# Optimization experiments

Measured on AMD Instinct MI355X. Metric: run time of the kernel, lower is better.

## Reference

```python
import jax, jax.numpy as jnp
import numpy as np

TEMP = 0.05
ALPHA = 0.1
EPS = 1e-12


def setup_inputs() -> dict:
    key = jax.random.key(0)
    k1, k2, k3, k4 = jax.random.split(key, 4)
    bs, emb_dim, n_class, n_aux = 16384, 512, 2000, 5
    features = jax.random.normal(k1, (bs, emb_dim), dtype=jnp.float32)
    word_embed = jax.random.normal(k2, (n_class, emb_dim), dtype=jnp.float32)
    label = jax.random.randint(k3, (bs,), 0, n_class)
    aux = jax.random.randint(k4, (bs, n_aux), 0, n_class)
    return {"features": features, "word_embed": word_embed, "label": label, "aux": aux}


def _cosine_logits(features, word_embed):
    # F.normalize(x, dim=-1): x / max(||x||, eps)
    f = features / jnp.maximum(jnp.linalg.norm(features, axis=-1, keepdims=True), EPS)
    w = word_embed / jnp.maximum(jnp.linalg.norm(word_embed, axis=-1, keepdims=True), EPS)
    return jnp.matmul(f, w.T) / TEMP  # (bs, n_class)


def reference(features, word_embed, label, aux):
    pred = _cosine_logits(features, word_embed)
    lse = jax.nn.logsumexp(pred, axis=1)                                  # log sum exp per row
    tgt = jnp.take_along_axis(pred, label[:, None], axis=1)[:, 0]         # pred[i, target[i]]
    # normal cross entropy: mean_i(-pred[i,t_i] + log sum exp(pred[i]))
    loss_normal = jnp.mean(-tgt + lse)
    # label-smoothing CE: -(1-a)*pred[i,t_i] + lse - (a/n_aux)*sum_j pred[i, aux[i,j]]
    single_alpha = ALPHA / aux.shape[-1]
    aux_logits = jnp.take_along_axis(pred, aux, axis=1)                   # (bs, n_aux)
    loss_ls = jnp.mean(-(1.0 - ALPHA) * tgt + lse - single_alpha * jnp.sum(aux_logits, axis=1))
    loss = 0.5 * (loss_normal + loss_ls)
    acc = jnp.mean((jnp.argmax(pred, axis=1) == label).astype(jnp.float32))
    return loss, acc
```

## Files before the change

kernel.cpp:

```cpp
#include <hip/hip_runtime.h>
#include <hip/hip_bf16.h>
#include <stdint.h>

#define BS   16384
#define NC   2000
#define NCP  2048
#define EMB  512
#define NAUX 5
#define NCHUNK 32
#define GBLK 4096

typedef __bf16 bf16x8 __attribute__((ext_vector_type(8)));
typedef float  f32x4  __attribute__((ext_vector_type(4)));

__global__ __launch_bounds__(256) void norm_kernel(
    const float* __restrict__ feat, const float* __restrict__ wemb,
    __bf16* __restrict__ fn, __bf16* __restrict__ wn)
{
    const int sub = threadIdx.x & 15;
    const int row = blockIdx.x * 16 + (threadIdx.x >> 4);

    if (row >= BS + NC) {
        bf16x8 z = {};
        bf16x8* d = (bf16x8*)(wn + (size_t)(row - BS) * EMB) + sub * 4;
        #pragma unroll
        for (int i = 0; i < 4; ++i) d[i] = z;
        return;
    }
    const float* src;
    __bf16* dst;
    if (row < BS) { src = feat + (size_t)row * EMB;        dst = fn + (size_t)row * EMB; }
    else          { src = wemb + (size_t)(row - BS) * EMB; dst = wn + (size_t)(row - BS) * EMB; }

    const float4* s4 = (const float4*)src + sub * 8;
    float4 x[8];
    float ss = 0.f;
    #pragma unroll
    for (int i = 0; i < 8; ++i) {
        x[i] = s4[i];
        ss += x[i].x * x[i].x + x[i].y * x[i].y + x[i].z * x[i].z + x[i].w * x[i].w;
    }
    #pragma unroll
    for (int m = 1; m < 16; m <<= 1) ss += __shfl_xor(ss, m, 64);
    const float scale = 1.0f / fmaxf(sqrtf(ss), 1e-12f);

    bf16x8* d = (bf16x8*)dst + sub * 4;
    #pragma unroll
    for (int i = 0; i < 4; ++i) {
        bf16x8 o;
        o[0] = (__bf16)(x[2*i].x   * scale); o[1] = (__bf16)(x[2*i].y   * scale);
        o[2] = (__bf16)(x[2*i].z   * scale); o[3] = (__bf16)(x[2*i].w   * scale);
        o[4] = (__bf16)(x[2*i+1].x * scale); o[5] = (__bf16)(x[2*i+1].y * scale);
        o[6] = (__bf16)(x[2*i+1].z * scale); o[7] = (__bf16)(x[2*i+1].w * scale);
        d[i] = o;
    }
}

__global__ __launch_bounds__(256) void main_kernel(
    const __bf16* __restrict__ fn, const __bf16* __restrict__ wn,
    float* __restrict__ es_part, unsigned* __restrict__ key_part)
{
    __shared__ __align__(16) __bf16 As[128 * 64];
    __shared__ __align__(16) __bf16 Bs[128 * 64];

    const int tid   = threadIdx.x;
    const int lane  = tid & 63;
    const int l15   = lane & 15;
    const int quad  = lane >> 4;
    const int wv    = tid >> 6;
    const int wvM   = wv >> 1;
    const int wvN   = wv & 1;
    const int xcd   = blockIdx.x & 7;
    const int j     = blockIdx.x >> 3;
    const int mTile = xcd * 16 + (j >> 4);
    const int nTile = j & 15;

    const __bf16* fbase = fn + (size_t)mTile * 128 * EMB;
    const __bf16* wbase = wn + (size_t)nTile * 128 * EMB;

    const int sRowIn = lane >> 3;
    const int sChunk = (lane & 7) ^ sRowIn;
    f32x4 acc[4][4] = {};

    for (int kk = 0; kk < EMB; kk += 64) {
        __syncthreads();
        #pragma unroll
        for (int p = 0; p < 4; ++p) {
            const int slot = wv * 4 + p;
            const size_t goff = (size_t)(slot * 8 + sRowIn) * EMB + kk + sChunk * 8;
            __builtin_amdgcn_global_load_lds(
                (const __attribute__((address_space(1))) void*)(fbase + goff),
                (__attribute__((address_space(3))) void*)(As + slot * 512), 16, 0, 0);
            __builtin_amdgcn_global_load_lds(
                (const __attribute__((address_space(1))) void*)(wbase + goff),
                (__attribute__((address_space(3))) void*)(Bs + slot * 512), 16, 0, 0);
        }
        __builtin_amdgcn_s_waitcnt(0);
        __syncthreads();

        #pragma unroll
        for (int kc = 0; kc < 2; ++kc) {
            bf16x8 aF[4], bF[4];
            #pragma unroll
            for (int i = 0; i < 4; ++i) {
                const int ar = wvM * 64 + i * 16 + l15;
                const int br = wvN * 64 + i * 16 + l15;
                const int ca = ((kc * 4 + quad) ^ (ar & 7)) * 8;
                const int cb = ((kc * 4 + quad) ^ (br & 7)) * 8;
                aF[i] = *(const bf16x8*)(As + ar * 64 + ca);
                bF[i] = *(const bf16x8*)(Bs + br * 64 + cb);
            }
            #pragma unroll
            for (int mi = 0; mi < 4; ++mi)
                #pragma unroll
                for (int ni = 0; ni < 4; ++ni)
                    acc[mi][ni] = __builtin_amdgcn_mfma_f32_16x16x32_bf16(
                        aF[mi], bF[ni], acc[mi][ni], 0, 0, 0);
        }
    }

    const float C20 = 28.853900817779268f;
    const int chunk = nTile * 2 + wvN;
    #pragma unroll
    for (int mi = 0; mi < 4; ++mi) {
        float    es[4] = {0.f, 0.f, 0.f, 0.f};
        unsigned km[4] = {0u, 0u, 0u, 0u};
        #pragma unroll
        for (int ni = 0; ni < 4; ++ni) {
            const int col = nTile * 128 + wvN * 64 + ni * 16 + l15;
            const unsigned colenc = 2047u - (unsigned)col;
            const bool valid = (col < NC);
            #pragma unroll
            for (int r = 0; r < 4; ++r) {
                float v = valid ? acc[mi][ni][r] : -3.0f;
                es[r] += exp2f((v - 1.0f) * C20);
                unsigned u = __float_as_uint(v);
                unsigned k = u ^ (unsigned)(((int)u >> 31) | 0x80000000);
                unsigned pk = (k & 0xFFFFF800u) | colenc;
                km[r] = pk > km[r] ? pk : km[r];
            }
        }
        #pragma unroll
        for (int r = 0; r < 4; ++r) {
            #pragma unroll
            for (int m = 1; m < 16; m <<= 1) {
                es[r] += __shfl_xor(es[r], m, 64);
                unsigned x = __shfl_xor(km[r], m, 64);
                km[r] = x > km[r] ? x : km[r];
            }
        }
        if (l15 == 0) {
            #pragma unroll
            for (int r = 0; r < 4; ++r) {
                const int row = mTile * 128 + wvM * 64 + mi * 16 + quad * 4 + r;
                es_part [chunk * BS + row] = es[r];
                key_part[chunk * BS + row] = km[r];
            }
        }
    }
}

__global__ __launch_bounds__(256) void gather_fin_kernel(
    const __bf16* __restrict__ fn, const __bf16* __restrict__ wn,
    const int* __restrict__ label, const int* __restrict__ aux,
    const float* __restrict__ es_part, const unsigned* __restrict__ key_part,
    float* __restrict__ blkpart)
{
    const int lane = threadIdx.x & 63;
    const int wv   = threadIdx.x >> 6;
    const int row  = blockIdx.x * 4 + wv;

    bf16x8 f8 = *((const bf16x8*)fn + (size_t)row * (EMB / 8) + lane);
    float fv[8];
    #pragma unroll
    for (int j = 0; j < 8; ++j) fv[j] = (float)f8[j];

    const int lab = label[row];
    int cols[6];
    cols[0] = lab;
    #pragma unroll
    for (int j = 0; j < NAUX; ++j) cols[j + 1] = aux[row * NAUX + j];

    float res[6];
    #pragma unroll
    for (int c = 0; c < 6; ++c) {
        bf16x8 w8 = *((const bf16x8*)wn + (size_t)cols[c] * (EMB / 8) + lane);
        float d = 0.f;
        #pragma unroll
        for (int j = 0; j < 8; ++j) d += fv[j] * (float)w8[j];
        #pragma unroll
        for (int m = 1; m < 64; m <<= 1) d += __shfl_xor(d, m, 64);
        res[c] = d;
    }
    const float tgt  = res[0] * 20.0f;
    const float auxs = (res[1] + res[2] + res[3] + res[4] + res[5]) * 20.0f;

    const int c = lane & 31;
    float    es = es_part [c * BS + row];
    unsigned k  = key_part[c * BS + row];
    #pragma unroll
    for (int m = 1; m < 32; m <<= 1) {
        es += __shfl_xor(es, m, 64);
        unsigned x = __shfl_xor(k, m, 64);
        k = x > k ? x : k;
    }
    const int amax = 2047 - (int)(k & 0x7FFu);
    const float loss = 20.0f + logf(es) - 0.95f * tgt - 0.01f * auxs;
    const float acc  = (amax == lab) ? 1.0f : 0.0f;

    __shared__ float sl[4], sa[4];
    if (lane == 0) { sl[wv] = loss; sa[wv] = acc; }
    __syncthreads();
    if (threadIdx.x == 0) {
        blkpart[blockIdx.x]        = sl[0] + sl[1] + sl[2] + sl[3];
        blkpart[GBLK + blockIdx.x] = sa[0] + sa[1] + sa[2] + sa[3];
    }
}

__global__ __launch_bounds__(256) void fin2_kernel(
    const float* __restrict__ blkpart, float* __restrict__ out)
{
    float l = 0.f, a = 0.f;
    for (int i = threadIdx.x; i < GBLK; i += 256) {
        l += blkpart[i];
        a += blkpart[GBLK + i];
    }
    #pragma unroll
    for (int m = 1; m < 64; m <<= 1) {
        l += __shfl_xor(l, m, 64);
        a += __shfl_xor(a, m, 64);
    }
    __shared__ float sl[4], sa[4];
    const int wv = threadIdx.x >> 6;
    if ((threadIdx.x & 63) == 0) { sl[wv] = l; sa[wv] = a; }
    __syncthreads();
    if (threadIdx.x == 0) {
        out[0] = (sl[0] + sl[1] + sl[2] + sl[3]) / (float)BS;
        out[1] = (sa[0] + sa[1] + sa[2] + sa[3]) / (float)BS;
    }
}

extern "C" void kernel_launch(void* const* d_in, const int* in_sizes, int n_in,
                              void* d_out, int out_size, void* d_ws, size_t ws_size,
                              hipStream_t stream)
{
    const float* feat  = (const float*)d_in[0];
    const float* wemb  = (const float*)d_in[1];
    const int*   label = (const int*)d_in[2];
    const int*   aux   = (const int*)d_in[3];

    char* ws = (char*)d_ws;
    __bf16*   fn      = (__bf16*)(ws);
    __bf16*   wn      = (__bf16*)(ws + 16777216);
    float*    es      = (float*)(ws + 18874368);
    unsigned* key     = (unsigned*)(ws + 20971520);
    float*    blkpart = (float*)(ws + 23068672);
    float*    out     = (float*)d_out;

    hipLaunchKernelGGL(norm_kernel, dim3((BS + NCP) / 16), dim3(256), 0, stream,
                       feat, wemb, fn, wn);
    hipLaunchKernelGGL(main_kernel, dim3((BS / 128) * (NCP / 128)), dim3(256), 0, stream,
                       fn, wn, es, key);
    hipLaunchKernelGGL(gather_fin_kernel, dim3(GBLK), dim3(256), 0, stream,
                       fn, wn, label, aux, es, key, blkpart);
    hipLaunchKernelGGL(fin2_kernel, dim3(1), dim3(256), 0, stream, blkpart, out);
}
```

Measured before the change: 161.8 us.

## Fuse target/aux logit gather into GEMM epilogue and merge final reductions

Computes the weighted target and aux logit sum inside the GEMM epilogue by comparing each column against the label and aux indices staged in shared memory. This removes the separate gather kernel that recomputed six dot products per row. The partial buffers switch to a row-major layout, and one small reduction kernel with atomic adds replaces the two-stage finish. The cost is extra compare and select work per accumulator element in the epilogue, one more partial buffer, and an added memset.

```diff
diff --git a/kernel.cpp b/kernel.cpp
--- a/kernel.cpp
+++ b/kernel.cpp
@@ -8,7 +8,6 @@
 #define EMB  512
 #define NAUX 5
 #define NCHUNK 32
-#define GBLK 4096
 
 typedef __bf16 bf16x8 __attribute__((ext_vector_type(8)));
 typedef float  f32x4  __attribute__((ext_vector_type(4)));
@@ -58,10 +57,14 @@
 
 __global__ __launch_bounds__(256) void main_kernel(
     const __bf16* __restrict__ fn, const __bf16* __restrict__ wn,
-    float* __restrict__ es_part, unsigned* __restrict__ key_part)
+    const int* __restrict__ label, const int* __restrict__ aux,
+    float* __restrict__ es_p, float* __restrict__ ta_p,
+    unsigned* __restrict__ key_p)
 {
     __shared__ __align__(16) __bf16 As[128 * 64];
     __shared__ __align__(16) __bf16 Bs[128 * 64];
+    __shared__ int lab_s[128];
+    __shared__ int aux_s[128 * NAUX];
 
     const int tid   = threadIdx.x;
     const int lane  = tid & 63;
@@ -74,8 +77,12 @@
     const int j     = blockIdx.x >> 3;
     const int mTile = xcd * 16 + (j >> 4);
     const int nTile = j & 15;
-
-    const __bf16* fbase = fn + (size_t)mTile * 128 * EMB;
+    const int mBase = mTile * 128;
+
+    if (tid < 128) lab_s[tid] = label[mBase + tid];
+    for (int i = tid; i < 128 * NAUX; i += 256) aux_s[i] = aux[(size_t)mBase * NAUX + i];
+
+    const __bf16* fbase = fn + (size_t)mBase * EMB;
     const __bf16* wbase = wn + (size_t)nTile * 128 * EMB;
 
     const int sRowIn = lane >> 3;
@@ -120,23 +127,33 @@
     }
 
     const float C20 = 28.853900817779268f;
-    const int chunk = nTile * 2 + wvN;
+    const int chunk   = nTile * 2 + wvN;
+    const int colBase = nTile * 128 + wvN * 64;
     #pragma unroll
     for (int mi = 0; mi < 4; ++mi) {
         float    es[4] = {0.f, 0.f, 0.f, 0.f};
+        float    ta[4] = {0.f, 0.f, 0.f, 0.f};
         unsigned km[4] = {0u, 0u, 0u, 0u};
         #pragma unroll
-        for (int ni = 0; ni < 4; ++ni) {
-            const int col = nTile * 128 + wvN * 64 + ni * 16 + l15;
-            const unsigned colenc = 2047u - (unsigned)col;
-            const bool valid = (col < NC);
-            #pragma unroll
-            for (int r = 0; r < 4; ++r) {
-                float v = valid ? acc[mi][ni][r] : -3.0f;
-                es[r] += exp2f((v - 1.0f) * C20);
-                unsigned u = __float_as_uint(v);
+        for (int r = 0; r < 4; ++r) {
+            const int rl  = wvM * 64 + mi * 16 + quad * 4 + r;
+            const int lab = lab_s[rl];
+            int ax[NAUX];
+            #pragma unroll
+            for (int q = 0; q < NAUX; ++q) ax[q] = aux_s[rl * NAUX + q];
+            #pragma unroll
+            for (int ni = 0; ni < 4; ++ni) {
+                const int col = colBase + ni * 16 + l15;
+                const float v = acc[mi][ni][r];
+                const float ve = (col < NC) ? v : -3.0f;
+                es[r] += exp2f((ve - 1.0f) * C20);
+                float w = (col == lab) ? 19.0f : 0.0f;
+                #pragma unroll
+                for (int q = 0; q < NAUX; ++q) w += (col == ax[q]) ? 0.2f : 0.0f;
+                ta[r] += v * w;
+                unsigned u = __float_as_uint(ve);
                 unsigned k = u ^ (unsigned)(((int)u >> 31) | 0x80000000);
-                unsigned pk = (k & 0xFFFFF800u) | colenc;
+                unsigned pk = (k & 0xFFFFF800u) | (2047u - (unsigned)col);
                 km[r] = pk > km[r] ? pk : km[r];
             }
         }
@@ -145,6 +162,7 @@
             #pragma unroll
             for (int m = 1; m < 16; m <<= 1) {
                 es[r] += __shfl_xor(es[r], m, 64);
+                ta[r] += __shfl_xor(ta[r], m, 64);
                 unsigned x = __shfl_xor(km[r], m, 64);
                 km[r] = x > km[r] ? x : km[r];
             }
@@ -152,91 +170,54 @@
         if (l15 == 0) {
             #pragma unroll
             for (int r = 0; r < 4; ++r) {
-                const int row = mTile * 128 + wvM * 64 + mi * 16 + quad * 4 + r;
-                es_part [chunk * BS + row] = es[r];
-                key_part[chunk * BS + row] = km[r];
-            }
-        }
-    }
-}
-
-__global__ __launch_bounds__(256) void gather_fin_kernel(
-    const __bf16* __restrict__ fn, const __bf16* __restrict__ wn,
-    const int* __restrict__ label, const int* __restrict__ aux,
-    const float* __restrict__ es_part, const unsigned* __restrict__ key_part,
-    float* __restrict__ blkpart)
+                const int row = mBase + wvM * 64 + mi * 16 + quad * 4 + r;
+                es_p [(size_t)row * NCHUNK + chunk] = es[r];
+                ta_p [(size_t)row * NCHUNK + chunk] = ta[r];
+                key_p[(size_t)row * NCHUNK + chunk] = km[r];
+            }
+        }
+    }
+}
+
+__global__ __launch_bounds__(256) void fin_kernel(
+    const float* __restrict__ es_p, const float* __restrict__ ta_p,
+    const unsigned* __restrict__ key_p, const int* __restrict__ label,
+    float* __restrict__ out)
 {
     const int lane = threadIdx.x & 63;
     const int wv   = threadIdx.x >> 6;
-    const int row  = blockIdx.x * 4 + wv;
-
-    bf16x8 f8 = *((const bf16x8*)fn + (size_t)row * (EMB / 8) + lane);
-    float fv[8];
-    #pragma unroll
-    for (int j = 0; j < 8; ++j) fv[j] = (float)f8[j];
-
-    const int lab = label[row];
-    int cols[6];
-    cols[0] = lab;
-    #pragma unroll
-    for (int j = 0; j < NAUX; ++j) cols[j + 1] = aux[row * NAUX + j];
-
-    float res[6];
-    #pragma unroll
-    for (int c = 0; c < 6; ++c) {
-        bf16x8 w8 = *((const bf16x8*)wn + (size_t)cols[c] * (EMB / 8) + lane);
-        float d = 0.f;
-        #pragma unroll
-        for (int j = 0; j < 8; ++j) d += fv[j] * (float)w8[j];
-        #pragma unroll
-        for (int m = 1; m < 64; m <<= 1) d += __shfl_xor(d, m, 64);
-        res[c] = d;
-    }
-    const float tgt  = res[0] * 20.0f;
-    const float auxs = (res[1] + res[2] + res[3] + res[4] + res[5]) * 20.0f;
-
-    const int c = lane & 31;
-    float    es = es_part [c * BS + row];
-    unsigned k  = key_part[c * BS + row];
-    #pragma unroll
-    for (int m = 1; m < 32; m <<= 1) {
-        es += __shfl_xor(es, m, 64);
-        unsigned x = __shfl_xor(k, m, 64);
-        k = x > k ? x : k;
-    }
-    const int amax = 2047 - (int)(k & 0x7FFu);
-    const float loss = 20.0f + logf(es) - 0.95f * tgt - 0.01f * auxs;
-    const float acc  = (amax == lab) ? 1.0f : 0.0f;
-
+    const int c    = lane & 31;
+    const int sub  = lane >> 5;
+
+    float lsum = 0.f, asum = 0.f;
+    for (int row = blockIdx.x * 8 + wv * 2 + sub; row < BS; row += 256 * 8) {
+        float    es = es_p [(size_t)row * NCHUNK + c];
+        float    ta = ta_p [(size_t)row * NCHUNK + c];
+        unsigned k  = key_p[(size_t)row * NCHUNK + c];
+        #pragma unroll
+        for (int m = 1; m < 32; m <<= 1) {
+            es += __shfl_xor(es, m, 64);
+            ta += __shfl_xor(ta, m, 64);
+            unsigned x = __shfl_xor(k, m, 64);
+            k = x > k ? x : k;
+        }
+        if (c == 0) {
+            const int amax = 2047 - (int)(k & 0x7FFu);
+            lsum += 20.0f + logf(es) - ta;
+            asum += (amax == label[row]) ? 1.0f : 0.0f;
+        }
+    }
+    #pragma unroll
+    for (int m = 1; m < 64; m <<= 1) {
+        lsum += __shfl_xor(lsum, m, 64);
+        asum += __shfl_xor(asum, m, 64);
+    }
     __shared__ float sl[4], sa[4];
-    if (lane == 0) { sl[wv] = loss; sa[wv] = acc; }
+    if (lane == 0) { sl[wv] = lsum; sa[wv] = asum; }
     __syncthreads();
     if (threadIdx.x == 0) {
-        blkpart[blockIdx.x]        = sl[0] + sl[1] + sl[2] + sl[3];
-        blkpart[GBLK + blockIdx.x] = sa[0] + sa[1] + sa[2] + sa[3];
-    }
-}
-
-__global__ __launch_bounds__(256) void fin2_kernel(
-    const float* __restrict__ blkpart, float* __restrict__ out)
-{
-    float l = 0.f, a = 0.f;
-    for (int i = threadIdx.x; i < GBLK; i += 256) {
-        l += blkpart[i];
-        a += blkpart[GBLK + i];
-    }
-    #pragma unroll
-    for (int m = 1; m < 64; m <<= 1) {
-        l += __shfl_xor(l, m, 64);
-        a += __shfl_xor(a, m, 64);
-    }
-    __shared__ float sl[4], sa[4];
-    const int wv = threadIdx.x >> 6;
-    if ((threadIdx.x & 63) == 0) { sl[wv] = l; sa[wv] = a; }
-    __syncthreads();
-    if (threadIdx.x == 0) {
-        out[0] = (sl[0] + sl[1] + sl[2] + sl[3]) / (float)BS;
-        out[1] = (sa[0] + sa[1] + sa[2] + sa[3]) / (float)BS;
+        atomicAdd(&out[0], (sl[0] + sl[1] + sl[2] + sl[3]) / (float)BS);
+        atomicAdd(&out[1], (sa[0] + sa[1] + sa[2] + sa[3]) / (float)BS);
     }
 }
 
@@ -250,18 +231,18 @@
     const int*   aux   = (const int*)d_in[3];
 
     char* ws = (char*)d_ws;
-    __bf16*   fn      = (__bf16*)(ws);
-    __bf16*   wn      = (__bf16*)(ws + 16777216);
-    float*    es      = (float*)(ws + 18874368);
-    unsigned* key     = (unsigned*)(ws + 20971520);
-    float*    blkpart = (float*)(ws + 23068672);
-    float*    out     = (float*)d_out;
-
+    __bf16*   fn    = (__bf16*)(ws);
+    __bf16*   wn    = (__bf16*)(ws + 16777216);
+    float*    es_p  = (float*)(ws + 18874368);
+    float*    ta_p  = (float*)(ws + 20971520);
+    unsigned* key_p = (unsigned*)(ws + 23068672);
+    float*    out   = (float*)d_out;
+
+    hipMemsetAsync(out, 0, 2 * sizeof(float), stream);
     hipLaunchKernelGGL(norm_kernel, dim3((BS + NCP) / 16), dim3(256), 0, stream,
                        feat, wemb, fn, wn);
     hipLaunchKernelGGL(main_kernel, dim3((BS / 128) * (NCP / 128)), dim3(256), 0, stream,
-                       fn, wn, es, key);
-    hipLaunchKernelGGL(gather_fin_kernel, dim3(GBLK), dim3(256), 0, stream,
-                       fn, wn, label, aux, es, key, blkpart);
-    hipLaunchKernelGGL(fin2_kernel, dim3(1), dim3(256), 0, stream, blkpart, out);
-}
+                       fn, wn, label, aux, es_p, ta_p, key_p);
+    hipLaunchKernelGGL(fin_kernel, dim3(256), dim3(256), 0, stream,
+                       es_p, ta_p, key_p, label, out);
+}
```

New measurement: 179.8 us. 1.11x slower.

## Restructure GEMM to keep full-K feature tile in LDS and stream weights directly

Applied to the files above, without the earlier changes.

The main GEMM kernel switches from a 128x128 tiled K-loop that stages both operands through LDS to a 64-row stripe whose full 512-wide feature slice is loaded into LDS once. Each wave now reads its 64 weight columns straight from global or L2 into registers, which removes the per-K-step barriers. The partial-result layout becomes row-major so the gather kernel reads each row's partials contiguously, and the final reduction kernel is replaced by float atomics into a memset output. The cost is heavier global traffic for weights without LDS reuse, launch bounds of 2 that may constrain registers, and nondeterministic atomic summation order.

```diff
diff --git a/kernel.cpp b/kernel.cpp
--- a/kernel.cpp
+++ b/kernel.cpp
@@ -8,7 +8,6 @@
 #define EMB  512
 #define NAUX 5
 #define NCHUNK 32
-#define GBLK 4096
 
 typedef __bf16 bf16x8 __attribute__((ext_vector_type(8)));
 typedef float  f32x4  __attribute__((ext_vector_type(4)));
@@ -56,78 +55,72 @@
     }
 }
 
-__global__ __launch_bounds__(256) void main_kernel(
+__global__ __launch_bounds__(256, 2) void main_kernel(
     const __bf16* __restrict__ fn, const __bf16* __restrict__ wn,
-    float* __restrict__ es_part, unsigned* __restrict__ key_part)
-{
-    __shared__ __align__(16) __bf16 As[128 * 64];
-    __shared__ __align__(16) __bf16 Bs[128 * 64];
-
-    const int tid   = threadIdx.x;
-    const int lane  = tid & 63;
-    const int l15   = lane & 15;
-    const int quad  = lane >> 4;
-    const int wv    = tid >> 6;
-    const int wvM   = wv >> 1;
-    const int wvN   = wv & 1;
-    const int xcd   = blockIdx.x & 7;
-    const int j     = blockIdx.x >> 3;
-    const int mTile = xcd * 16 + (j >> 4);
-    const int nTile = j & 15;
-
-    const __bf16* fbase = fn + (size_t)mTile * 128 * EMB;
-    const __bf16* wbase = wn + (size_t)nTile * 128 * EMB;
-
-    const int sRowIn = lane >> 3;
-    const int sChunk = (lane & 7) ^ sRowIn;
+    float* __restrict__ es_p, unsigned* __restrict__ key_p)
+{
+    __shared__ __align__(16) __bf16 As[64 * 512];
+
+    const int tid    = threadIdx.x;
+    const int lane   = tid & 63;
+    const int l15    = lane & 15;
+    const int quad   = lane >> 4;
+    const int wv     = tid >> 6;
+    const int xcd    = blockIdx.x & 7;
+    const int idx    = blockIdx.x >> 3;
+    const int stripe = xcd * 32 + (idx >> 3);
+    const int nsplit = idx & 7;
+    const int mBase  = stripe * 64;
+    const int colBase = nsplit * 256 + wv * 64;
+
+    #pragma unroll
+    for (int p = 0; p < 2; ++p) {
+        const int row = (tid >> 3) + p * 32;
+        const __bf16* g = fn + (size_t)(mBase + row) * EMB;
+        #pragma unroll
+        for (int i = 0; i < 8; ++i) {
+            const int c  = (tid & 7) + i * 8;
+            const int cp = c ^ (row & 7);
+            *(bf16x8*)(As + row * 512 + cp * 8) = *(const bf16x8*)(g + c * 8);
+        }
+    }
+    __syncthreads();
+
     f32x4 acc[4][4] = {};
-
-    for (int kk = 0; kk < EMB; kk += 64) {
-        __syncthreads();
-        #pragma unroll
-        for (int p = 0; p < 4; ++p) {
-            const int slot = wv * 4 + p;
-            const size_t goff = (size_t)(slot * 8 + sRowIn) * EMB + kk + sChunk * 8;
-            __builtin_amdgcn_global_load_lds(
-                (const __attribute__((address_space(1))) void*)(fbase + goff),
-                (__attribute__((address_space(3))) void*)(As + slot * 512), 16, 0, 0);
-            __builtin_amdgcn_global_load_lds(
-                (const __attribute__((address_space(1))) void*)(wbase + goff),
-                (__attribute__((address_space(3))) void*)(Bs + slot * 512), 16, 0, 0);
-        }
-        __builtin_amdgcn_s_waitcnt(0);
-        __syncthreads();
-
-        #pragma unroll
-        for (int kc = 0; kc < 2; ++kc) {
-            bf16x8 aF[4], bF[4];
-            #pragma unroll
-            for (int i = 0; i < 4; ++i) {
-                const int ar = wvM * 64 + i * 16 + l15;
-                const int br = wvN * 64 + i * 16 + l15;
-                const int ca = ((kc * 4 + quad) ^ (ar & 7)) * 8;
-                const int cb = ((kc * 4 + quad) ^ (br & 7)) * 8;
-                aF[i] = *(const bf16x8*)(As + ar * 64 + ca);
-                bF[i] = *(const bf16x8*)(Bs + br * 64 + cb);
-            }
-            #pragma unroll
-            for (int mi = 0; mi < 4; ++mi)
-                #pragma unroll
-                for (int ni = 0; ni < 4; ++ni)
-                    acc[mi][ni] = __builtin_amdgcn_mfma_f32_16x16x32_bf16(
-                        aF[mi], bF[ni], acc[mi][ni], 0, 0, 0);
-        }
+    const bf16x8* bp[4];
+    #pragma unroll
+    for (int ni = 0; ni < 4; ++ni)
+        bp[ni] = (const bf16x8*)(wn + (size_t)(colBase + ni * 16 + l15) * EMB) + quad;
+
+    #pragma unroll
+    for (int kc = 0; kc < 16; ++kc) {
+        bf16x8 bF[4], aF[4];
+        #pragma unroll
+        for (int ni = 0; ni < 4; ++ni)
+            bF[ni] = bp[ni][kc * 4];
+        #pragma unroll
+        for (int mi = 0; mi < 4; ++mi) {
+            const int row = mi * 16 + l15;
+            const int c   = (kc * 4 + quad) ^ (row & 7);
+            aF[mi] = *(const bf16x8*)(As + row * 512 + c * 8);
+        }
+        #pragma unroll
+        for (int mi = 0; mi < 4; ++mi)
+            #pragma unroll
+            for (int ni = 0; ni < 4; ++ni)
+                acc[mi][ni] = __builtin_amdgcn_mfma_f32_16x16x32_bf16(
+                    aF[mi], bF[ni], acc[mi][ni], 0, 0, 0);
     }
 
     const float C20 = 28.853900817779268f;
-    const int chunk = nTile * 2 + wvN;
+    const int chunk = nsplit * 4 + wv;
     #pragma unroll
     for (int mi = 0; mi < 4; ++mi) {
         float    es[4] = {0.f, 0.f, 0.f, 0.f};
         unsigned km[4] = {0u, 0u, 0u, 0u};
         #pragma unroll
         for (int ni = 0; ni < 4; ++ni) {
-            const int col = nTile * 128 + wvN * 64 + ni * 16 + l15;
+            const int col = colBase + ni * 16 + l15;
             const unsigned colenc = 2047u - (unsigned)col;
             const bool valid = (col < NC);
             #pragma unroll
@@ -152,9 +145,9 @@
         if (l15 == 0) {
             #pragma unroll
             for (int r = 0; r < 4; ++r) {
-                const int row = mTile * 128 + wvM * 64 + mi * 16 + quad * 4 + r;
-                es_part [chunk * BS + row] = es[r];
-                key_part[chunk * BS + row] = km[r];
+                const int row = mBase + mi * 16 + quad * 4 + r;
+                es_p [(size_t)row * NCHUNK + chunk] = es[r];
+                key_p[(size_t)row * NCHUNK + chunk] = km[r];
             }
         }
     }
@@ -163,8 +156,8 @@
 __global__ __launch_bounds__(256) void gather_fin_kernel(
     const __bf16* __restrict__ fn, const __bf16* __restrict__ wn,
     const int* __restrict__ label, const int* __restrict__ aux,
-    const float* __restrict__ es_part, const unsigned* __restrict__ key_part,
-    float* __restrict__ blkpart)
+    const float* __restrict__ es_p, const unsigned* __restrict__ key_p,
+    float* __restrict__ out)
 {
     const int lane = threadIdx.x & 63;
     const int wv   = threadIdx.x >> 6;
@@ -196,8 +189,8 @@
     const float auxs = (res[1] + res[2] + res[3] + res[4] + res[5]) * 20.0f;
 
     const int c = lane & 31;
-    float    es = es_part [c * BS + row];
-    unsigned k  = key_part[c * BS + row];
+    float    es = es_p [(size_t)row * NCHUNK + c];
+    unsigned k  = key_p[(size_t)row * NCHUNK + c];
     #pragma unroll
     for (int m = 1; m < 32; m <<= 1) {
         es += __shfl_xor(es, m, 64);
@@ -212,31 +205,8 @@
     if (lane == 0) { sl[wv] = loss; sa[wv] = acc; }
     __syncthreads();
     if (threadIdx.x == 0) {
-        blkpart[blockIdx.x]        = sl[0] + sl[1] + sl[2] + sl[3];
-        blkpart[GBLK + blockIdx.x] = sa[0] + sa[1] + sa[2] + sa[3];
-    }
-}
-
-__global__ __launch_bounds__(256) void fin2_kernel(
-    const float* __restrict__ blkpart, float* __restrict__ out)
-{
-    float l = 0.f, a = 0.f;
-    for (int i = threadIdx.x; i < GBLK; i += 256) {
-        l += blkpart[i];
-        a += blkpart[GBLK + i];
-    }
-    #pragma unroll
-    for (int m = 1; m < 64; m <<= 1) {
-        l += __shfl_xor(l, m, 64);
-        a += __shfl_xor(a, m, 64);
-    }
-    __shared__ float sl[4], sa[4];
-    const int wv = threadIdx.x >> 6;
-    if ((threadIdx.x & 63) == 0) { sl[wv] = l; sa[wv] = a; }
-    __syncthreads();
-    if (threadIdx.x == 0) {
-        out[0] = (sl[0] + sl[1] + sl[2] + sl[3]) / (float)BS;
-        out[1] = (sa[0] + sa[1] + sa[2] + sa[3]) / (float)BS;
+        atomicAdd(&out[0], (sl[0] + sl[1] + sl[2] + sl[3]) / (float)BS);
+        atomicAdd(&out[1], (sa[0] + sa[1] + sa[2] + sa[3]) / (float)BS);
     }
 }
 
@@ -250,18 +220,17 @@
     const int*   aux   = (const int*)d_in[3];
 
     char* ws = (char*)d_ws;
-    __bf16*   fn      = (__bf16*)(ws);
-    __bf16*   wn      = (__bf16*)(ws + 16777216);
-    float*    es      = (float*)(ws + 18874368);
-    unsigned* key     = (unsigned*)(ws + 20971520);
-    float*    blkpart = (float*)(ws + 23068672);
-    float*    out     = (float*)d_out;
-
+    __bf16*   fn    = (__bf16*)(ws);
+    __bf16*   wn    = (__bf16*)(ws + 16777216);
+    float*    es_p  = (float*)(ws + 18874368);
+    unsigned* key_p = (unsigned*)(ws + 20971520);
+    float*    out   = (float*)d_out;
+
+    hipMemsetAsync(out, 0, 2 * sizeof(float), stream);
     hipLaunchKernelGGL(norm_kernel, dim3((BS + NCP) / 16), dim3(256), 0, stream,
                        feat, wemb, fn, wn);
-    hipLaunchKernelGGL(main_kernel, dim3((BS / 128) * (NCP / 128)), dim3(256), 0, stream,
-                       fn, wn, es, key);
-    hipLaunchKernelGGL(gather_fin_kernel, dim3(GBLK), dim3(256), 0, stream,
-                       fn, wn, label, aux, es, key, blkpart);
-    hipLaunchKernelGGL(fin2_kernel, dim3(1), dim3(256), 0, stream, blkpart, out);
-}
+    hipLaunchKernelGGL(main_kernel, dim3((BS / 64) * 8), dim3(256), 0, stream,
+                       fn, wn, es_p, key_p);
+    hipLaunchKernelGGL(gather_fin_kernel, dim3(BS / 4), dim3(256), 0, stream,
+                       fn, wn, label, aux, es_p, key_p, out);
+}
```

Measured after the change: 273.8 us. 1.69x slower.
